# Kernel tuning notes

Measured on AMD Instinct MI355X. Metric: run time of the kernel, lower is better.

## Reference

```python
import jax, jax.numpy as jnp
import numpy as np

INT_MIN, INT_MAX = -128.0, 127.0   # signed 8-bit weight range
UINT_MAX = 255.0                   # unsigned 8-bit activation range


def weight_quant(W):
    """Int8 per-tensor fixed-point (power-of-two scale from max-abs stats), STE."""
    max_abs = jax.lax.stop_gradient(jnp.max(jnp.abs(W)))
    # restrict threshold to power of two (ceil), scale = 2^e / 2^(bw-1)
    exp = jnp.ceil(jnp.log2(jnp.maximum(max_abs, 1e-12)))
    scale = jnp.exp2(exp) / 128.0
    q = jnp.clip(jnp.round(W / scale), INT_MIN, INT_MAX) * scale
    return W + jax.lax.stop_gradient(q - W)


def act_quant_relu(x, scale):
    """QuantReLU: relu then unsigned 8-bit quant-dequant with per-tensor scale, STE."""
    x = jax.nn.relu(x)
    s = jax.lax.stop_gradient(scale)
    q = jnp.clip(jnp.round(x / s), 0.0, UINT_MAX) * s
    return x + jax.lax.stop_gradient(q - x)


def setup_inputs() -> dict:
    key = jax.random.key(0)
    ks = jax.random.split(key, 9)
    B, D, U = 500000, 256, 64
    x = jax.random.normal(ks[0], (B, D), dtype=jnp.float32)
    W1 = jax.random.normal(ks[1], (U, D), dtype=jnp.float32) * (1.0 / np.sqrt(D))
    b1 = jax.random.normal(ks[2], (U,), dtype=jnp.float32) * 0.01
    W2 = jax.random.normal(ks[3], (U, U), dtype=jnp.float32) * (1.0 / np.sqrt(U))
    b2 = jax.random.normal(ks[4], (U,), dtype=jnp.float32) * 0.01
    Wout = jax.random.normal(ks[5], (1, U), dtype=jnp.float32) * (1.0 / np.sqrt(U))
    bout = jax.random.normal(ks[6], (1,), dtype=jnp.float32) * 0.01
    a1 = jax.random.uniform(ks[7], (), dtype=jnp.float32, minval=0.01, maxval=0.1)
    a2 = jax.random.uniform(ks[8], (), dtype=jnp.float32, minval=0.01, maxval=0.1)
    return {"x": x, "W1": W1, "b1": b1, "W2": W2, "b2": b2,
            "Wout": Wout, "bout": bout, "a1": a1, "a2": a2}


def reference(x, W1, b1, W2, b2, Wout, bout, a1, a2):
    # layer 1: quant-linear -> QuantReLU (dropout is identity at inference)
    h = x @ weight_quant(W1).T + b1
    h = act_quant_relu(h, a1)
    # layer 2
    h = h @ weight_quant(W2).T + b2
    h = act_quant_relu(h, a2)
    # output quant-linear (no activation quant)
    return h @ weight_quant(Wout).T + bout
```

## Files before the change

### kernel.cpp

```cpp
#include <hip/hip_runtime.h>

typedef __attribute__((ext_vector_type(8))) short s16x8;
typedef __attribute__((ext_vector_type(4))) float f32x4;

union FragU {
    unsigned int u[4];
    uint4 v;
    s16x8 s;
};

__device__ __forceinline__ float pow2_scale_inv(float ma, float& scale) {
    ma = fmaxf(ma, 1e-12f);
    unsigned u = __float_as_uint(ma);
    int E = (int)((u >> 23) & 255u);
    int ce = ((u & 0x7fffffu) == 0u) ? (E - 127) : (E - 126);
    int se = ce - 7;
    scale = __uint_as_float((unsigned)(se + 127) << 23);
    return __uint_as_float((unsigned)(127 - se) << 23);
}

__device__ __forceinline__ unsigned pack_hi16(unsigned u0, unsigned u1) {
    return __builtin_amdgcn_perm(u1, u0, 0x07060302u);
}

__device__ __forceinline__ float uni(float x) {
    return __uint_as_float((unsigned)__builtin_amdgcn_readfirstlane(__float_as_uint(x)));
}

__global__ __launch_bounds__(512, 4) void fused_kernel(
    const float* __restrict__ x,
    const float* __restrict__ W1,
    const float* __restrict__ b1,
    const float* __restrict__ W2,
    const float* __restrict__ b2,
    const float* __restrict__ Wo,
    const float* __restrict__ boutp,
    const float* __restrict__ a1p,
    const float* __restrict__ a2p,
    float* __restrict__ out,
    int ntiles) {

    __shared__ __align__(16) unsigned short w1f[16384];
    __shared__ __align__(16) unsigned short w2f[4096];
    __shared__ __align__(16) unsigned short stg[8][1024];
    __shared__ float redm[24];

    const int t = threadIdx.x;
    const int lane = t & 63;
    const int wv = t >> 6;

    float m1 = 0.f, m2 = 0.f, mo = 0.f;
    #pragma unroll 4
    for (int k = 0; k < 8; ++k) {
        float4 v = *(const float4*)(W1 + 4 * (t + 512 * k));
        m1 = fmaxf(m1, fmaxf(fmaxf(fabsf(v.x), fabsf(v.y)),
                             fmaxf(fabsf(v.z), fabsf(v.w))));
    }
    #pragma unroll
    for (int k = 0; k < 2; ++k) {
        float4 v = *(const float4*)(W2 + 4 * (t + 512 * k));
        m2 = fmaxf(m2, fmaxf(fmaxf(fabsf(v.x), fabsf(v.y)),
                             fmaxf(fabsf(v.z), fabsf(v.w))));
    }
    if (t < 64) mo = fabsf(Wo[t]);

    #pragma unroll
    for (int m = 1; m < 64; m <<= 1) {
        m1 = fmaxf(m1, __shfl_xor(m1, m, 64));
        m2 = fmaxf(m2, __shfl_xor(m2, m, 64));
        mo = fmaxf(mo, __shfl_xor(mo, m, 64));
    }
    if (lane == 0) { redm[wv] = m1; redm[8 + wv] = m2; redm[16 + wv] = mo; }
    __syncthreads();
    m1 = fmaxf(fmaxf(fmaxf(redm[0], redm[1]), fmaxf(redm[2], redm[3])),
               fmaxf(fmaxf(redm[4], redm[5]), fmaxf(redm[6], redm[7])));
    m2 = fmaxf(fmaxf(fmaxf(redm[8], redm[9]), fmaxf(redm[10], redm[11])),
               fmaxf(fmaxf(redm[12], redm[13]), fmaxf(redm[14], redm[15])));
    mo = fmaxf(fmaxf(fmaxf(redm[16], redm[17]), fmaxf(redm[18], redm[19])),
               fmaxf(fmaxf(redm[20], redm[21]), fmaxf(redm[22], redm[23])));

    float s1v, s2v, sov;
    const float i1 = uni(pow2_scale_inv(m1, s1v));
    const float i2 = uni(pow2_scale_inv(m2, s2v));
    const float io = uni(pow2_scale_inv(mo, sov));
    const float s1 = uni(s1v);

    const float a1 = uni(a1p[0]), a2 = uni(a2p[0]);
    const double d1 = 1.0 / (double)a1;
    const float i1h = uni((float)d1), i1l = uni((float)(d1 - (double)(float)d1));
    const double d2 = 1.0 / (double)a2;
    const float i2h = uni((float)d2), i2l = uni((float)(d2 - (double)(float)d2));

    #pragma unroll 4
    for (int k = 0; k < 8; ++k) {
        const int i0 = 4 * (t + 512 * k);
        float4 v = *(const float4*)(W1 + i0);
        float q4[4] = {v.x, v.y, v.z, v.w};
        #pragma unroll
        for (int e = 0; e < 4; ++e) {
            const int i = i0 + e;
            float q = fminf(fmaxf(rintf(q4[e] * i1), -128.f), 127.f);
            const int u = i >> 8, kk = i & 255;
            const int c = u >> 4, ccb = u & 15, s = kk >> 5, gg = (kk >> 3) & 3, j = kk & 7;
            w1f[((s * 4 + c) * 64 + gg * 16 + ccb) * 8 + j] =
                (unsigned short)(__float_as_uint(q) >> 16);
        }
    }
    #pragma unroll
    for (int k = 0; k < 2; ++k) {
        const int i0 = 4 * (t + 512 * k);
        float4 v = *(const float4*)(W2 + i0);
        float q4[4] = {v.x, v.y, v.z, v.w};
        #pragma unroll
        for (int e = 0; e < 4; ++e) {
            const int i = i0 + e;
            float q = fminf(fmaxf(rintf(q4[e] * i2), -128.f), 127.f);
            const int vv = i >> 6, kk = i & 63;
            const int c = vv >> 4, ccb = vv & 15, s = kk >> 5, gg = (kk >> 3) & 3, j = kk & 7;
            w2f[((s * 4 + c) * 64 + gg * 16 + ccb) * 8 + j] =
                (unsigned short)(__float_as_uint(q) >> 16);
        }
    }
    __syncthreads();

    const float boutv = uni(boutp[0]);
    const float c21 = uni(a1 * s2v);
    const float c3  = uni(a2 * sov);

    const int cc = lane & 15;
    const int g  = lane >> 4;

    float b1c[4], b2c[4], wqc[4];
    #pragma unroll
    for (int c = 0; c < 4; ++c) {
        b1c[c] = b1[c * 16 + cc];
        b2c[c] = b2[c * 16 + cc];
        wqc[c] = fminf(fmaxf(rintf(Wo[c * 16 + cc] * io), -128.f), 127.f);
    }

    unsigned short* st = stg[wv];

    const int b = blockIdx.x;
    const int nb = gridDim.x;
    const int pb = (nb & 7) ? b : ((b & 7) * (nb >> 3) + (b >> 3));
    const int S = (int)(((long long)pb * ntiles) / nb);
    const int E = (int)(((long long)(pb + 1) * ntiles) / nb);
    const int t0 = S + wv;

    float4 xv[8];
    if (t0 < E) {
        const float* xp0 = x + (size_t)(t0 * 16 + cc) * 256 + g * 8;
        #pragma unroll
        for (int s = 0; s < 4; ++s) {
            xv[2 * s]     = *(const float4*)(xp0 + s * 32);
            xv[2 * s + 1] = *(const float4*)(xp0 + s * 32 + 4);
        }
    }

    for (int tile = t0; tile < E; tile += 8) {
        const float* xp = x + (size_t)(tile * 16 + cc) * 256 + g * 8;
        const int nt = tile + 8;
        const bool pf = nt < E;
        const float* xpn = pf ? (x + (size_t)(nt * 16 + cc) * 256 + g * 8) : xp;

        f32x4 acc[4];
        #pragma unroll
        for (int c = 0; c < 4; ++c) acc[c] = (f32x4){0.f, 0.f, 0.f, 0.f};

        #pragma unroll
        for (int ks = 0; ks < 8; ++ks) {
            const int sl = ks & 3;
            const float4 A = xv[2 * sl];
            const float4 B = xv[2 * sl + 1];

            const float* pb_ = (ks < 4) ? (xp + (ks + 4) * 32) : (xpn + (ks - 4) * 32);
            xv[2 * sl]     = *(const float4*)(pb_);
            xv[2 * sl + 1] = *(const float4*)(pb_ + 4);

            float f[8] = {A.x, A.y, A.z, A.w, B.x, B.y, B.z, B.w};
            FragU hi, lo, lo2;
            #pragma unroll
            for (int p = 0; p < 4; ++p) {
                const float f0 = f[2 * p], f1 = f[2 * p + 1];
                const unsigned u0 = __float_as_uint(f0), u1 = __float_as_uint(f1);
                hi.u[p] = pack_hi16(u0, u1);
                const float r0 = f0 - __uint_as_float(u0 & 0xffff0000u);
                const float r1 = f1 - __uint_as_float(u1 & 0xffff0000u);
                const unsigned v0 = __float_as_uint(r0), v1 = __float_as_uint(r1);
                lo.u[p] = pack_hi16(v0, v1);
                const float q0 = r0 - __uint_as_float(v0 & 0xffff0000u);
                const float q1 = r1 - __uint_as_float(v1 & 0xffff0000u);
                lo2.u[p] = pack_hi16(__float_as_uint(q0), __float_as_uint(q1));
            }
            #pragma unroll
            for (int c = 0; c < 4; ++c) {
                FragU bb;
                bb.v = *(const uint4*)&w1f[((ks * 4 + c) * 64 + lane) * 8];
                acc[c] = __builtin_amdgcn_mfma_f32_16x16x32_bf16(hi.s,  bb.s, acc[c], 0, 0, 0);
                acc[c] = __builtin_amdgcn_mfma_f32_16x16x32_bf16(lo.s,  bb.s, acc[c], 0, 0, 0);
                acc[c] = __builtin_amdgcn_mfma_f32_16x16x32_bf16(lo2.s, bb.s, acc[c], 0, 0, 0);
            }
        }

        #pragma unroll
        for (int c = 0; c < 4; ++c) {
            #pragma unroll
            for (int j = 0; j < 4; ++j) {
                float h = fmaf(acc[c][j], s1, b1c[c]);
                h = fmaxf(h, 0.f);
                float n = rintf(fmaf(h, i1l, h * i1h));
                n = fminf(n, 255.f);
                const int r = g * 4 + j;
                const int u = c * 16 + cc;
                const int pos = ((u >> 5) * 64 + ((u >> 3) & 3) * 16 + r) * 8 + (u & 7);
                st[pos] = (unsigned short)(__float_as_uint(n) >> 16);
            }
        }
        asm volatile("s_waitcnt lgkmcnt(0)" ::: "memory");

        s16x8 afrag[2];
        #pragma unroll
        for (int s = 0; s < 2; ++s) {
            FragU a;
            a.v = *(const uint4*)&st[(s * 64 + lane) * 8];
            afrag[s] = a.s;
        }

        f32x4 acc2[4];
        #pragma unroll
        for (int c = 0; c < 4; ++c) acc2[c] = (f32x4){0.f, 0.f, 0.f, 0.f};
        #pragma unroll
        for (int s = 0; s < 2; ++s) {
            #pragma unroll
            for (int c = 0; c < 4; ++c) {
                FragU bb;
                bb.v = *(const uint4*)&w2f[((s * 4 + c) * 64 + lane) * 8];
                acc2[c] = __builtin_amdgcn_mfma_f32_16x16x32_bf16(afrag[s], bb.s, acc2[c], 0, 0, 0);
            }
        }

        float psum[4] = {0.f, 0.f, 0.f, 0.f};
        #pragma unroll
        for (int c = 0; c < 4; ++c) {
            #pragma unroll
            for (int j = 0; j < 4; ++j) {
                float h = fmaf(acc2[c][j], c21, b2c[c]);
                h = fmaxf(h, 0.f);
                float n = rintf(fmaf(h, i2l, h * i2h));
                n = fminf(n, 255.f);
                psum[j] = fmaf(n, wqc[c], psum[j]);
            }
        }
        #pragma unroll
        for (int j = 0; j < 4; ++j) {
            #pragma unroll
            for (int mask = 1; mask < 16; mask <<= 1)
                psum[j] += __shfl_xor(psum[j], mask, 16);
        }

        if (cc == 0) {
            float4 o;
            o.x = fmaf(psum[0], c3, boutv);
            o.y = fmaf(psum[1], c3, boutv);
            o.z = fmaf(psum[2], c3, boutv);
            o.w = fmaf(psum[3], c3, boutv);
            *(float4*)(out + (size_t)tile * 16 + g * 4) = o;
        }
    }
}

extern "C" void kernel_launch(void* const* d_in, const int* in_sizes, int n_in,
                              void* d_out, int out_size, void* d_ws, size_t ws_size,
                              hipStream_t stream) {
    const float* x    = (const float*)d_in[0];
    const float* W1   = (const float*)d_in[1];
    const float* b1   = (const float*)d_in[2];
    const float* W2   = (const float*)d_in[3];
    const float* b2   = (const float*)d_in[4];
    const float* Wout = (const float*)d_in[5];
    const float* bout = (const float*)d_in[6];
    const float* a1   = (const float*)d_in[7];
    const float* a2   = (const float*)d_in[8];
    float* out = (float*)d_out;

    const int rows = in_sizes[0] / 256;
    const int ntiles = rows / 16;

    int blocks = 512;
    if (blocks * 8 > ntiles) blocks = (ntiles + 7) / 8;
    fused_kernel<<<blocks, 512, 0, stream>>>(x, W1, b1, W2, b2, Wout, bout,
                                             a1, a2, out, ntiles);
}
```

Measured before the change: 107.8 us.

## Stream x tiles into swizzled LDS via direct global-to-LDS loads

Replaces register-based prefetch of input rows with per-wave `global_load_lds` DMA into a swizzled LDS buffer. The next tile's load is issued after the first-layer MFMAs, then waited on at the end of the iteration. Blocks shrink from 512 to 256 threads, the grid from 512 to 256 blocks, and each wave now strides by 4 tiles. This aims to cut VGPR pressure and the cost of staging x in registers, but it greatly lowers resident waves per CU and leaves only single-tile lookahead to hide memory latency.

```diff
diff --git a/kernel.cpp b/kernel.cpp
--- a/kernel.cpp
+++ b/kernel.cpp
@@ -27,7 +27,7 @@
     return __uint_as_float((unsigned)__builtin_amdgcn_readfirstlane(__float_as_uint(x)));
 }
 
-__global__ __launch_bounds__(512, 4) void fused_kernel(
+__global__ __launch_bounds__(256, 1) void fused_kernel(
     const float* __restrict__ x,
     const float* __restrict__ W1,
     const float* __restrict__ b1,
@@ -42,8 +42,9 @@
 
     __shared__ __align__(16) unsigned short w1f[16384];
     __shared__ __align__(16) unsigned short w2f[4096];
-    __shared__ __align__(16) unsigned short stg[8][1024];
-    __shared__ float redm[24];
+    __shared__ __align__(16) unsigned short stg[4][1024];
+    __shared__ __align__(16) unsigned int   xbuf[4][4096];
+    __shared__ float redm[12];
 
     const int t = threadIdx.x;
     const int lane = t & 63;
@@ -51,14 +52,14 @@
 
     float m1 = 0.f, m2 = 0.f, mo = 0.f;
     #pragma unroll 4
-    for (int k = 0; k < 8; ++k) {
-        float4 v = *(const float4*)(W1 + 4 * (t + 512 * k));
+    for (int k = 0; k < 16; ++k) {
+        float4 v = *(const float4*)(W1 + 4 * (t + 256 * k));
         m1 = fmaxf(m1, fmaxf(fmaxf(fabsf(v.x), fabsf(v.y)),
                              fmaxf(fabsf(v.z), fabsf(v.w))));
     }
     #pragma unroll
-    for (int k = 0; k < 2; ++k) {
-        float4 v = *(const float4*)(W2 + 4 * (t + 512 * k));
+    for (int k = 0; k < 4; ++k) {
+        float4 v = *(const float4*)(W2 + 4 * (t + 256 * k));
         m2 = fmaxf(m2, fmaxf(fmaxf(fabsf(v.x), fabsf(v.y)),
                              fmaxf(fabsf(v.z), fabsf(v.w))));
     }
@@ -70,14 +71,11 @@
         m2 = fmaxf(m2, __shfl_xor(m2, m, 64));
         mo = fmaxf(mo, __shfl_xor(mo, m, 64));
     }
-    if (lane == 0) { redm[wv] = m1; redm[8 + wv] = m2; redm[16 + wv] = mo; }
+    if (lane == 0) { redm[wv] = m1; redm[4 + wv] = m2; redm[8 + wv] = mo; }
     __syncthreads();
-    m1 = fmaxf(fmaxf(fmaxf(redm[0], redm[1]), fmaxf(redm[2], redm[3])),
-               fmaxf(fmaxf(redm[4], redm[5]), fmaxf(redm[6], redm[7])));
-    m2 = fmaxf(fmaxf(fmaxf(redm[8], redm[9]), fmaxf(redm[10], redm[11])),
-               fmaxf(fmaxf(redm[12], redm[13]), fmaxf(redm[14], redm[15])));
-    mo = fmaxf(fmaxf(fmaxf(redm[16], redm[17]), fmaxf(redm[18], redm[19])),
-               fmaxf(fmaxf(redm[20], redm[21]), fmaxf(redm[22], redm[23])));
+    m1 = fmaxf(fmaxf(redm[0], redm[1]), fmaxf(redm[2], redm[3]));
+    m2 = fmaxf(fmaxf(redm[4], redm[5]), fmaxf(redm[6], redm[7]));
+    mo = fmaxf(fmaxf(redm[8], redm[9]), fmaxf(redm[10], redm[11]));
 
     float s1v, s2v, sov;
     const float i1 = uni(pow2_scale_inv(m1, s1v));
@@ -92,8 +90,8 @@
     const float i2h = uni((float)d2), i2l = uni((float)(d2 - (double)(float)d2));
 
     #pragma unroll 4
-    for (int k = 0; k < 8; ++k) {
-        const int i0 = 4 * (t + 512 * k);
+    for (int k = 0; k < 16; ++k) {
+        const int i0 = 4 * (t + 256 * k);
         float4 v = *(const float4*)(W1 + i0);
         float q4[4] = {v.x, v.y, v.z, v.w};
         #pragma unroll
@@ -107,8 +105,8 @@
         }
     }
     #pragma unroll
-    for (int k = 0; k < 2; ++k) {
-        const int i0 = 4 * (t + 512 * k);
+    for (int k = 0; k < 4; ++k) {
+        const int i0 = 4 * (t + 256 * k);
         float4 v = *(const float4*)(W2 + i0);
         float q4[4] = {v.x, v.y, v.z, v.w};
         #pragma unroll
@@ -140,6 +138,11 @@
 
     unsigned short* st = stg[wv];
 
+    const char* xbc = (const char*)xbuf[wv];
+    const char* xr0 = xbc + cc * 1024 + (((2 * g + 0 + cc) & 7) << 4);
+    const char* xr1 = xbc + cc * 1024 + (((2 * g + 1 + cc) & 7) << 4);
+    const int lreg = (lane >> 3) << 7;
+
     const int b = blockIdx.x;
     const int nb = gridDim.x;
     const int pb = (nb & 7) ? b : ((b & 7) * (nb >> 3) + (b >> 3));
@@ -147,21 +150,22 @@
     const int E = (int)(((long long)(pb + 1) * ntiles) / nb);
     const int t0 = S + wv;
 
-    float4 xv[8];
     if (t0 < E) {
-        const float* xp0 = x + (size_t)(t0 * 16 + cc) * 256 + g * 8;
-        #pragma unroll
-        for (int s = 0; s < 4; ++s) {
-            xv[2 * s]     = *(const float4*)(xp0 + s * 32);
-            xv[2 * s + 1] = *(const float4*)(xp0 + s * 32 + 4);
-        }
-    }
-
-    for (int tile = t0; tile < E; tile += 8) {
-        const float* xp = x + (size_t)(tile * 16 + cc) * 256 + g * 8;
-        const int nt = tile + 8;
-        const bool pf = nt < E;
-        const float* xpn = pf ? (x + (size_t)(nt * 16 + cc) * 256 + g * 8) : xp;
+        const char* gs = (const char*)(x + (size_t)t0 * 4096);
+        #pragma unroll
+        for (int r = 0; r < 16; ++r) {
+            const int so = lreg + (((lane - r) & 7) << 4);
+            __builtin_amdgcn_global_load_lds(
+                (const unsigned int*)(gs + r * 1024 + so),
+                &xbuf[wv][r * 256], 16, 0, 0);
+        }
+    }
+    asm volatile("s_waitcnt vmcnt(0)" ::: "memory");
+    __builtin_amdgcn_sched_barrier(0);
+
+    for (int tile = t0; tile < E; tile += 4) {
+        const int nt = tile + 4;
+        const bool hasnext = nt < E;
 
         f32x4 acc[4];
         #pragma unroll
@@ -169,13 +173,8 @@
 
         #pragma unroll
         for (int ks = 0; ks < 8; ++ks) {
-            const int sl = ks & 3;
-            const float4 A = xv[2 * sl];
-            const float4 B = xv[2 * sl + 1];
-
-            const float* pb_ = (ks < 4) ? (xp + (ks + 4) * 32) : (xpn + (ks - 4) * 32);
-            xv[2 * sl]     = *(const float4*)(pb_);
-            xv[2 * sl + 1] = *(const float4*)(pb_ + 4);
+            const float4 A = *(const float4*)(xr0 + ks * 128);
+            const float4 B = *(const float4*)(xr1 + ks * 128);
 
             float f[8] = {A.x, A.y, A.z, A.w, B.x, B.y, B.z, B.w};
             FragU hi, lo, lo2;
@@ -202,6 +201,20 @@
             }
         }
 
+        asm volatile("s_waitcnt lgkmcnt(0)" ::: "memory");
+        __builtin_amdgcn_sched_barrier(0);
+        if (hasnext) {
+            const char* gs = (const char*)(x + (size_t)nt * 4096);
+            #pragma unroll
+            for (int r = 0; r < 16; ++r) {
+                const int so = lreg + (((lane - r) & 7) << 4);
+                __builtin_amdgcn_global_load_lds(
+                    (const unsigned int*)(gs + r * 1024 + so),
+                    &xbuf[wv][r * 256], 16, 0, 0);
+            }
+        }
+        __builtin_amdgcn_sched_barrier(0);
+
         #pragma unroll
         for (int c = 0; c < 4; ++c) {
             #pragma unroll
@@ -266,6 +279,9 @@
             o.w = fmaf(psum[3], c3, boutv);
             *(float4*)(out + (size_t)tile * 16 + g * 4) = o;
         }
+
+        asm volatile("s_waitcnt vmcnt(1)" ::: "memory");
+        __builtin_amdgcn_sched_barrier(0);
     }
 }
 
@@ -286,8 +302,8 @@
     const int rows = in_sizes[0] / 256;
     const int ntiles = rows / 16;
 
-    int blocks = 512;
-    if (blocks * 8 > ntiles) blocks = (ntiles + 7) / 8;
-    fused_kernel<<<blocks, 512, 0, stream>>>(x, W1, b1, W2, b2, Wout, bout,
+    int blocks = 256;
+    if (blocks * 4 > ntiles) blocks = (ntiles + 3) / 4;
+    fused_kernel<<<blocks, 256, 0, stream>>>(x, W1, b1, W2, b2, Wout, bout,
                                              a1, a2, out, ntiles);
 }
```

Result: slower. 130.2 us (+20.7%).
